# Performance work log

Hardware: AMD Instinct MI355X
Metric: run time of the kernel (lower is better)

The kernel has to match this reference:

```python
import jax, jax.numpy as jnp
import numpy as np

GAMMA = 20.0
GAMMA2 = 10.0
KATZ_FACTOR = 0.999
EPS = 1e-12


def setup_inputs() -> dict:
    key = jax.random.key(0)
    k1, k2 = jax.random.split(key)
    b, n_way, k_shot, q, c, h, w = 32, 5, 5, 75, 640, 5, 5
    support_xf = jax.random.normal(k1, (b, n_way * k_shot, c, h, w), dtype=jnp.float32)
    query_xf = jax.random.normal(k2, (b, q, c, h, w), dtype=jnp.float32)
    return {"support_xf": support_xf, "query_xf": query_xf, "n_way": n_way, "k_shot": k_shot}


def _l2norm(x, axis):
    return x * jax.lax.rsqrt(jnp.sum(x * x, axis=axis, keepdims=True) + EPS)


def reference(support_xf, query_xf, n_way, k_shot):
    b, s, c, h, w = support_xf.shape
    q = query_xf.shape[1]
    hw = h * w
    # prototype support features: mean over shots -> (b, n_way, c, hw)
    sup = support_xf.reshape(b, n_way, k_shot, c, hw).mean(axis=2)
    qry = query_xf.reshape(b, q, c, hw)
    # cosine similarity between every query location and every support location
    sup_n = _l2norm(sup, axis=2)   # (b, n, c, hw)
    qry_n = _l2norm(qry, axis=2)   # (b, q, c, hw)
    # S[b,q,i,n,k]: query pos i vs support (class n, pos k) -> (b*q, M_q, M_s)
    M_q, M_s = hw, n_way * hw
    N = b * q
    S = jnp.einsum('bqci,bnck->bqink', qry_n, sup_n).reshape(N, M_q, M_s)
    # double softmax transition blocks
    T_sq = jax.nn.softmax(GAMMA * S, axis=-1)                    # (N, M_q, M_s)
    T_qs = jax.nn.softmax(GAMMA2 * S.transpose(0, 2, 1), axis=-1)  # (N, M_s, M_q)
    # bipartite block transition matrix T (N, M_s+M_q, M_s+M_q)
    top = jnp.concatenate(
        [jnp.zeros((N, M_s, M_s), S.dtype), T_sq.transpose(0, 2, 1)], axis=-1)
    bot = jnp.concatenate(
        [T_qs.transpose(0, 2, 1), jnp.zeros((N, M_q, M_q), S.dtype)], axis=-1)
    T = jnp.concatenate([top, bot], axis=-2)
    M = M_s + M_q
    eye = jnp.eye(M, dtype=S.dtype)
    ones = jnp.ones((N, M, 1), S.dtype)
    # katz = (inv(I - kT) - I) @ 1 == solve(I - kT, 1) - 1
    katz = (jnp.linalg.solve(eye[None] - KATZ_FACTOR * T, ones) - ones).squeeze(-1)
    kq = katz[:, M_s:]
    ks = katz[:, :M_s]
    katz_query = kq / kq.sum(-1, keepdims=True)
    katz_support = ks / ks.sum(-1, keepdims=True)
    katz_support = katz_support.reshape(b, q, n_way, hw)
    katz_support = katz_support / katz_support.sum(-1, keepdims=True)
    katz_support = katz_support.reshape(b, q, n_way, 1, h, w)
    katz_query = katz_query.reshape(b, q, 1, h, w)
    return (katz_query, katz_support)
```

## Files before the change

### kernel.cpp

```cpp
#include <hip/hip_runtime.h>

namespace {
constexpr int CH = 640, HW = 25, MS = 125;
constexpr int CHW = CH * HW;
constexpr float GAMMA = 20.f, GAMMA2 = 10.f;
constexpr float EPS = 1e-12f;
}

__global__ __launch_bounds__(256)
void prep_sup_kernel(const float* __restrict__ sup, float* __restrict__ sup_t) {
  __shared__ __align__(16) float m[CHW];
  __shared__ float inv[HW];
  const int bn = blockIdx.x;
  const float* base = sup + (size_t)(bn / 5) * (25 * CHW)
                          + (size_t)(bn % 5) * (5 * CHW);
  for (int idx = threadIdx.x; idx < CHW; idx += 256) {
    float s = 0.f;
    #pragma unroll
    for (int sh = 0; sh < 5; ++sh) s += base[sh * CHW + idx];
    m[idx] = s * 0.2f;
  }
  __syncthreads();
  {
    int i = threadIdx.x >> 3, s8 = threadIdx.x & 7;
    if (i < HW) {
      float p = 0.f;
      for (int c = s8; c < CH; c += 8) { float v = m[c * HW + i]; p += v * v; }
      p += __shfl_xor(p, 1); p += __shfl_xor(p, 2); p += __shfl_xor(p, 4);
      if (s8 == 0) inv[i] = rsqrtf(p + EPS);
    }
  }
  __syncthreads();
  float* outp = sup_t + (size_t)bn * CHW;
  for (int idx = threadIdx.x; idx < CHW; idx += 256) {
    int k = idx / CH, c = idx - k * CH;
    outp[idx] = m[c * HW + k] * inv[k];
  }
}

__global__ __launch_bounds__(256)
void gemm_s_kernel(const float* __restrict__ qry, const float* __restrict__ sup_t,
                   float* __restrict__ Sout) {
  __shared__ __align__(16) float pool[4224];
  __shared__ float invq_s[128];
  float* atile = pool;
  float* btile = pool + 2112;

  const int tid = threadIdx.x;
  const int Bl = (blockIdx.x & 7) * 60 + (blockIdx.x >> 3);
  const int b = Bl / 15, qg = Bl - 15 * b;
  const float* qbase = qry + ((size_t)b * 75 + (size_t)qg * 5) * CHW;
  const float* sbase = sup_t + (size_t)b * (MS * CH);
  const int ty = tid >> 4, tx = tid & 15;

  float acc[2][2][4][4];
  #pragma unroll
  for (int g = 0; g < 2; ++g)
    #pragma unroll
    for (int h = 0; h < 2; ++h)
      #pragma unroll
      for (int u = 0; u < 4; ++u)
        #pragma unroll
        for (int v = 0; v < 4; ++v) acc[g][h][u][v] = 0.f;
  float npart = 0.f;

  for (int c0 = 0; c0 < CH; c0 += 16) {
    __syncthreads();
    #pragma unroll
    for (int mm = 0; mm < 8; ++mm) {
      int idx = tid + 256 * mm;
      int k = idx >> 7, row = idx & 127;
      float v = 0.f;
      if (row < MS) {
        int qq = row / 25, i = row - 25 * qq;
        v = qbase[(size_t)qq * CHW + (size_t)(c0 + k) * 25 + i];
      }
      atile[k * 132 + row] = v;
    }
    #pragma unroll
    for (int mm = 0; mm < 2; ++mm) {
      int idx = tid + 256 * mm;
      int col = idx >> 2, kq = idx & 3;
      float4 v = make_float4(0.f, 0.f, 0.f, 0.f);
      if (col < MS) v = *(const float4*)(sbase + (size_t)col * CH + c0 + 4 * kq);
      btile[(4 * kq + 0) * 132 + col] = v.x;
      btile[(4 * kq + 1) * 132 + col] = v.y;
      btile[(4 * kq + 2) * 132 + col] = v.z;
      btile[(4 * kq + 3) * 132 + col] = v.w;
    }
    __syncthreads();
    if (tid < MS) {
      #pragma unroll
      for (int k = 0; k < 16; ++k) { float v = atile[k * 132 + tid]; npart += v * v; }
    }
    #pragma unroll
    for (int k = 0; k < 16; ++k) {
      const float4 a0 = *(const float4*)&atile[k * 132 + 4 * ty];
      const float4 a1 = *(const float4*)&atile[k * 132 + 64 + 4 * ty];
      const float4 b0 = *(const float4*)&btile[k * 132 + 4 * tx];
      const float4 b1 = *(const float4*)&btile[k * 132 + 64 + 4 * tx];
      const float ag[2][4] = {{a0.x, a0.y, a0.z, a0.w}, {a1.x, a1.y, a1.z, a1.w}};
      const float bg[2][4] = {{b0.x, b0.y, b0.z, b0.w}, {b1.x, b1.y, b1.z, b1.w}};
      #pragma unroll
      for (int g = 0; g < 2; ++g)
        #pragma unroll
        for (int u = 0; u < 4; ++u)
          #pragma unroll
          for (int h = 0; h < 2; ++h)
            #pragma unroll
            for (int v = 0; v < 4; ++v) acc[g][h][u][v] += ag[g][u] * bg[h][v];
    }
  }
  if (tid < MS) invq_s[tid] = rsqrtf(npart + EPS);
  __syncthreads();

  float* Sg = Sout + (size_t)(b * 75 + qg * 5) * 3200;
  #pragma unroll
  for (int g = 0; g < 2; ++g)
    #pragma unroll
    for (int u = 0; u < 4; ++u) {
      const int row = g * 64 + 4 * ty + u;
      if (row < MS) {
        const float iv = invq_s[row];
        const int qq = row / 25, r = row - 25 * qq;
        #pragma unroll
        for (int h = 0; h < 2; ++h) {
          float4 val;
          val.x = acc[g][h][u][0] * iv;
          val.y = acc[g][h][u][1] * iv;
          val.z = acc[g][h][u][2] * iv;
          val.w = acc[g][h][u][3] * iv;
          *(float4*)(Sg + (size_t)qq * 3200 + r * 128 + h * 64 + 4 * tx) = val;
        }
      }
    }
}

__global__ __launch_bounds__(256)
void solve_kernel(const float* __restrict__ Sg, float* __restrict__ out) {
  __shared__ float Sld[25 * 131];
  __shared__ float Qm[3125];
  __shared__ double Msol[675];
  __shared__ double xsd[HW];
  __shared__ float kqs[HW];
  __shared__ float ksf[MS];

  const int tid = threadIdx.x;
  const int bq = blockIdx.x;
  const float* src = Sg + (size_t)bq * 3200;
  for (int idx = tid; idx < 3200; idx += 256) {
    const int row = idx >> 7, c = idx & 127;
    Sld[row * 131 + c] = src[idx];
  }
  __syncthreads();

  if (tid < MS) {
    float mx = -1e30f;
    #pragma unroll
    for (int i = 0; i < HW; ++i) mx = fmaxf(mx, Sld[i * 131 + tid]);
    float e[HW]; float sum = 0.f;
    #pragma unroll
    for (int i = 0; i < HW; ++i) { e[i] = __expf(GAMMA2 * (Sld[i * 131 + tid] - mx)); sum += e[i]; }
    float is = 1.f / sum;
    #pragma unroll
    for (int i = 0; i < HW; ++i) Qm[tid * HW + i] = e[i] * is;
  }
  __syncthreads();

  {
    int i = tid >> 3, s8 = tid & 7;
    if (i < HW) {
      float mx = -1e30f;
      for (int j = s8; j < MS; j += 8) mx = fmaxf(mx, Sld[i * 131 + j]);
      mx = fmaxf(mx, __shfl_xor(mx, 1));
      mx = fmaxf(mx, __shfl_xor(mx, 2));
      mx = fmaxf(mx, __shfl_xor(mx, 4));
      float sum = 0.f;
      for (int j = s8; j < MS; j += 8) {
        float e = __expf(GAMMA * (Sld[i * 131 + j] - mx));
        Sld[i * 131 + j] = e; sum += e;
      }
      sum += __shfl_xor(sum, 1); sum += __shfl_xor(sum, 2); sum += __shfl_xor(sum, 4);
      float is = 1.f / sum;
      for (int j = s8; j < MS; j += 8) Sld[i * 131 + j] *= is;
    }
  }
  __syncthreads();

  #pragma unroll
  for (int t = 0; t < 3; ++t) {
    const int pp = tid + 256 * t;
    if (pp < 650) {
      const int i = pp / 26, i2 = pp - 26 * i;
      float s = 0.f;
      if (i2 < 25) {
        for (int j = 0; j < MS; ++j) s += Qm[j * HW + i] * Sld[i2 * 131 + j];
        Msol[i * 27 + i2] = (i == i2 ? 1.0 : 0.0) - 0.998001 * (double)s;
      } else {
        for (int j = 0; j < MS; ++j) s += Qm[j * HW + i];
        Msol[i * 27 + 25] = 1.0 + 0.999 * (double)s;
      }
    }
  }
  __syncthreads();

  for (int k = 0; k < 24; ++k) {
    const double invp = 1.0 / Msol[k * 27 + k];
    const int jj = k + 1 + (tid & 31);
    for (int i = k + 1 + (tid >> 5); i < HW; i += 8) {
      const double f = Msol[i * 27 + k] * invp;
      if (jj <= HW) Msol[i * 27 + jj] -= f * Msol[k * 27 + jj];
    }
    __syncthreads();
  }
  for (int k = 24; k >= 0; --k) {
    const double xk = Msol[k * 27 + 25] / Msol[k * 27 + k];
    if (tid == 0) xsd[k] = xk;
    if (tid < k) Msol[tid * 27 + 25] -= Msol[tid * 27 + k] * xk;
    __syncthreads();
  }

  if (tid < HW) kqs[tid] = (float)(xsd[tid] - 1.0);
  if (tid < MS) {
    float a = 0.f;
    #pragma unroll
    for (int i = 0; i < HW; ++i) a += Sld[i * 131 + tid] * (float)xsd[i];
    ksf[tid] = 0.999f * a;
  }
  __syncthreads();
  if (tid < HW) {
    float s = 0.f;
    #pragma unroll
    for (int i = 0; i < HW; ++i) s += kqs[i];
    out[(size_t)bq * HW + tid] = kqs[tid] / s;
  }
  if (tid < MS) {
    const int n = tid / HW;
    float s = 0.f;
    #pragma unroll
    for (int k2 = 0; k2 < HW; ++k2) s += ksf[n * HW + k2];
    out[60000 + (size_t)bq * MS + tid] = ksf[tid] / s;
  }
}

__global__ __launch_bounds__(256)
void melmask_kernel(const float* __restrict__ qry, const float* __restrict__ sup_t,
                    float* __restrict__ out) {
  __shared__ __align__(16) float pool[4224];
  __shared__ __align__(16) float Sld[3125];
  __shared__ double Msol[675];
  __shared__ double xsd[HW];
  __shared__ float invq_s[128];
  __shared__ float kqs[HW];
  __shared__ float ksf[MS];

  float* atile = pool;
  float* btile = pool + 2112;
  float* Qm    = pool;

  const int tid = threadIdx.x;
  const int Bl = (blockIdx.x & 7) * 60 + (blockIdx.x >> 3);
  const int b = Bl / 15, qg = Bl - 15 * b;
  const float* qbase = qry + ((size_t)b * 75 + (size_t)qg * 5) * CHW;
  const float* sbase = sup_t + (size_t)b * (MS * CH);
  const int ty = tid >> 4, tx = tid & 15;

  float acc[2][2][4][4];
  #pragma unroll
  for (int g = 0; g < 2; ++g)
    #pragma unroll
    for (int h = 0; h < 2; ++h)
      #pragma unroll
      for (int u = 0; u < 4; ++u)
        #pragma unroll
        for (int v = 0; v < 4; ++v) acc[g][h][u][v] = 0.f;
  float npart = 0.f;

  for (int c0 = 0; c0 < CH; c0 += 16) {
    __syncthreads();
    #pragma unroll
    for (int mm = 0; mm < 8; ++mm) {
      int idx = tid + 256 * mm;
      int k = idx >> 7, row = idx & 127;
      float v = 0.f;
      if (row < MS) {
        int qq = row / 25, i = row - 25 * qq;
        v = qbase[(size_t)qq * CHW + (size_t)(c0 + k) * 25 + i];
      }
      atile[k * 132 + row] = v;
    }
    #pragma unroll
    for (int mm = 0; mm < 2; ++mm) {
      int idx = tid + 256 * mm;
      int col = idx >> 2, kq = idx & 3;
      float4 v = make_float4(0.f, 0.f, 0.f, 0.f);
      if (col < MS) v = *(const float4*)(sbase + (size_t)col * CH + c0 + 4 * kq);
      btile[(4 * kq + 0) * 132 + col] = v.x;
      btile[(4 * kq + 1) * 132 + col] = v.y;
      btile[(4 * kq + 2) * 132 + col] = v.z;
      btile[(4 * kq + 3) * 132 + col] = v.w;
    }
    __syncthreads();
    if (tid < MS) {
      #pragma unroll
      for (int k = 0; k < 16; ++k) { float v = atile[k * 132 + tid]; npart += v * v; }
    }
    #pragma unroll
    for (int k = 0; k < 16; ++k) {
      const float4 a0 = *(const float4*)&atile[k * 132 + 4 * ty];
      const float4 a1 = *(const float4*)&atile[k * 132 + 64 + 4 * ty];
      const float4 b0 = *(const float4*)&btile[k * 132 + 4 * tx];
      const float4 b1 = *(const float4*)&btile[k * 132 + 64 + 4 * tx];
      const float ag[2][4] = {{a0.x, a0.y, a0.z, a0.w}, {a1.x, a1.y, a1.z, a1.w}};
      const float bg[2][4] = {{b0.x, b0.y, b0.z, b0.w}, {b1.x, b1.y, b1.z, b1.w}};
      #pragma unroll
      for (int g = 0; g < 2; ++g)
        #pragma unroll
        for (int u = 0; u < 4; ++u)
          #pragma unroll
          for (int h = 0; h < 2; ++h)
            #pragma unroll
            for (int v = 0; v < 4; ++v) acc[g][h][u][v] += ag[g][u] * bg[h][v];
    }
  }
  if (tid < MS) invq_s[tid] = rsqrtf(npart + EPS);
  __syncthreads();

  for (int qq = 0; qq < 5; ++qq) {
    const int bq = b * 75 + qg * 5 + qq;
    const int r0 = qq * 25;
    #pragma unroll
    for (int g = 0; g < 2; ++g)
      #pragma unroll
      for (int u = 0; u < 4; ++u) {
        const int row = g * 64 + 4 * ty + u;
        if (row >= r0 && row < r0 + 25) {
          const int r = row - r0;
          const float iv = invq_s[row];
          #pragma unroll
          for (int h = 0; h < 2; ++h)
            #pragma unroll
            for (int v = 0; v < 4; ++v) {
              const int col = h * 64 + 4 * tx + v;
              if (col < MS) Sld[r * MS + col] = acc[g][h][u][v] * iv;
            }
        }
      }
    __syncthreads();
    if (tid < MS) {
      float mx = -1e30f;
      #pragma unroll
      for (int i = 0; i < HW; ++i) mx = fmaxf(mx, Sld[i * MS + tid]);
      float e[HW]; float sum = 0.f;
      #pragma unroll
      for (int i = 0; i < HW; ++i) { e[i] = __expf(GAMMA2 * (Sld[i * MS + tid] - mx)); sum += e[i]; }
      float is = 1.f / sum;
      #pragma unroll
      for (int i = 0; i < HW; ++i) Qm[tid * HW + i] = e[i] * is;
    }
    __syncthreads();
    {
      int i = tid >> 3, s8 = tid & 7;
      if (i < HW) {
        float mx = -1e30f;
        for (int j = s8; j < MS; j += 8) mx = fmaxf(mx, Sld[i * MS + j]);
        mx = fmaxf(mx, __shfl_xor(mx, 1));
        mx = fmaxf(mx, __shfl_xor(mx, 2));
        mx = fmaxf(mx, __shfl_xor(mx, 4));
        float sum = 0.f;
        for (int j = s8; j < MS; j += 8) {
          float e = __expf(GAMMA * (Sld[i * MS + j] - mx));
          Sld[i * MS + j] = e; sum += e;
        }
        sum += __shfl_xor(sum, 1); sum += __shfl_xor(sum, 2); sum += __shfl_xor(sum, 4);
        float is = 1.f / sum;
        for (int j = s8; j < MS; j += 8) Sld[i * MS + j] *= is;
      }
    }
    __syncthreads();
    float* P = Sld;
    #pragma unroll
    for (int t = 0; t < 3; ++t) {
      const int pp = tid + 256 * t;
      if (pp < 650) {
        const int i = pp / 26, i2 = pp - 26 * i;
        float s = 0.f;
        if (i2 < 25) {
          for (int j = 0; j < MS; ++j) s += Qm[j * HW + i] * P[i2 * MS + j];
          Msol[i * 27 + i2] = (i == i2 ? 1.0 : 0.0) - 0.998001 * (double)s;
        } else {
          for (int j = 0; j < MS; ++j) s += Qm[j * HW + i];
          Msol[i * 27 + 25] = 1.0 + 0.999 * (double)s;
        }
      }
    }
    __syncthreads();
    for (int k = 0; k < 24; ++k) {
      const double invp = 1.0 / Msol[k * 27 + k];
      const int jj = k + 1 + (tid & 31);
      for (int i = k + 1 + (tid >> 5); i < HW; i += 8) {
        const double f = Msol[i * 27 + k] * invp;
        if (jj <= HW) Msol[i * 27 + jj] -= f * Msol[k * 27 + jj];
      }
      __syncthreads();
    }
    for (int k = 24; k >= 0; --k) {
      const double xk = Msol[k * 27 + 25] / Msol[k * 27 + k];
      if (tid == 0) xsd[k] = xk;
      if (tid < k) Msol[tid * 27 + 25] -= Msol[tid * 27 + k] * xk;
      __syncthreads();
    }
    if (tid < HW) kqs[tid] = (float)(xsd[tid] - 1.0);
    if (tid < MS) {
      float a = 0.f;
      #pragma unroll
      for (int i = 0; i < HW; ++i) a += P[i * MS + tid] * (float)xsd[i];
      ksf[tid] = 0.999f * a;
    }
    __syncthreads();
    if (tid < HW) {
      float s = 0.f;
      #pragma unroll
      for (int i = 0; i < HW; ++i) s += kqs[i];
      out[(size_t)bq * HW + tid] = kqs[tid] / s;
    }
    if (tid < MS) {
      const int n = tid / HW;
      float s = 0.f;
      #pragma unroll
      for (int k2 = 0; k2 < HW; ++k2) s += ksf[n * HW + k2];
      out[60000 + (size_t)bq * MS + tid] = ksf[tid] / s;
    }
    __syncthreads();
  }
}

extern "C" void kernel_launch(void* const* d_in, const int* in_sizes, int n_in,
                              void* d_out, int out_size, void* d_ws, size_t ws_size,
                              hipStream_t stream) {
  const float* sup = (const float*)d_in[0];
  const float* qry = (const float*)d_in[1];
  float* outp = (float*)d_out;
  float* sup_t = (float*)d_ws;
  prep_sup_kernel<<<160, 256, 0, stream>>>(sup, sup_t);
  const size_t need = 10240000ull + (size_t)2400 * 3200 * 4;
  if (ws_size >= need) {
    float* Sg = (float*)((char*)d_ws + 10240000);
    gemm_s_kernel<<<480, 256, 0, stream>>>(qry, sup_t, Sg);
    solve_kernel<<<2400, 256, 0, stream>>>(Sg, outp);
  } else {
    melmask_kernel<<<480, 256, 0, stream>>>(qry, sup_t, outp);
  }
}
```

Baseline: 260.7 us.

## Double-buffer GEMM tiles via direct global-to-LDS loads with padded support layout

Adds a support-prep kernel that writes the normalized support as a channel-major, 128-column padded array, so B tiles can be copied with 16-byte direct global-to-LDS loads. The GEMM kernel now double-buffers its A and B tiles in shared memory and prefetches the next channel chunk with global_load_lds while computing the current one. This is meant to overlap global memory latency with FMA work and to remove the register round-trip and transpose stores. The cost is doubled LDS use, which may lower occupancy. A rows beyond 124 are clamped and load duplicate data instead of zeros, which affects only the unused padded rows.

```diff
diff --git a/kernel.cpp b/kernel.cpp
--- a/kernel.cpp
+++ b/kernel.cpp
@@ -8,12 +8,12 @@
 }
 
 __global__ __launch_bounds__(256)
-void prep_sup_kernel(const float* __restrict__ sup, float* __restrict__ sup_t) {
+void prep_sup128_kernel(const float* __restrict__ sup, float* __restrict__ supt) {
   __shared__ __align__(16) float m[CHW];
   __shared__ float inv[HW];
   const int bn = blockIdx.x;
-  const float* base = sup + (size_t)(bn / 5) * (25 * CHW)
-                          + (size_t)(bn % 5) * (5 * CHW);
+  const int b = bn / 5, n = bn % 5;
+  const float* base = sup + ((size_t)b * 25 + n * 5) * CHW;
   for (int idx = threadIdx.x; idx < CHW; idx += 256) {
     float s = 0.f;
     #pragma unroll
@@ -31,6 +31,40 @@
     }
   }
   __syncthreads();
+  float* ob = supt + (size_t)b * (CH * 128);
+  for (int idx = threadIdx.x; idx < CHW; idx += 256) {
+    int c = idx / 25, i = idx - c * 25;
+    ob[c * 128 + n * 25 + i] = m[idx] * inv[i];
+  }
+  if (n == 0)
+    for (int c = threadIdx.x; c < CH; c += 256) {
+      ob[c * 128 + 125] = 0.f; ob[c * 128 + 126] = 0.f; ob[c * 128 + 127] = 0.f;
+    }
+}
+
+__global__ __launch_bounds__(256)
+void prep_sup_kernel(const float* __restrict__ sup, float* __restrict__ sup_t) {
+  __shared__ __align__(16) float m[CHW];
+  __shared__ float inv[HW];
+  const int bn = blockIdx.x;
+  const float* base = sup + (size_t)(bn / 5) * (25 * CHW) + (size_t)(bn % 5) * (5 * CHW);
+  for (int idx = threadIdx.x; idx < CHW; idx += 256) {
+    float s = 0.f;
+    #pragma unroll
+    for (int sh = 0; sh < 5; ++sh) s += base[sh * CHW + idx];
+    m[idx] = s * 0.2f;
+  }
+  __syncthreads();
+  {
+    int i = threadIdx.x >> 3, s8 = threadIdx.x & 7;
+    if (i < HW) {
+      float p = 0.f;
+      for (int c = s8; c < CH; c += 8) { float v = m[c * HW + i]; p += v * v; }
+      p += __shfl_xor(p, 1); p += __shfl_xor(p, 2); p += __shfl_xor(p, 4);
+      if (s8 == 0) inv[i] = rsqrtf(p + EPS);
+    }
+  }
+  __syncthreads();
   float* outp = sup_t + (size_t)bn * CHW;
   for (int idx = threadIdx.x; idx < CHW; idx += 256) {
     int k = idx / CH, c = idx - k * CH;
@@ -39,19 +73,49 @@
 }
 
 __global__ __launch_bounds__(256)
-void gemm_s_kernel(const float* __restrict__ qry, const float* __restrict__ sup_t,
+void gemm_s_kernel(const float* __restrict__ qry, const float* __restrict__ sup128,
                    float* __restrict__ Sout) {
-  __shared__ __align__(16) float pool[4224];
+  __shared__ __align__(16) float atile[2][16 * 128];
+  __shared__ __align__(16) float btile[2][16 * 128];
   __shared__ float invq_s[128];
-  float* atile = pool;
-  float* btile = pool + 2112;
 
   const int tid = threadIdx.x;
+  const int wid = tid >> 6, lane = tid & 63;
   const int Bl = (blockIdx.x & 7) * 60 + (blockIdx.x >> 3);
   const int b = Bl / 15, qg = Bl - 15 * b;
   const float* qbase = qry + ((size_t)b * 75 + (size_t)qg * 5) * CHW;
-  const float* sbase = sup_t + (size_t)b * (MS * CH);
+  const float* sb = sup128 + (size_t)b * (CH * 128);
   const int ty = tid >> 4, tx = tid & 15;
+
+  const int row0 = lane;
+  const int qq0 = row0 / 25, i0 = row0 - 25 * qq0;
+  int row1 = 64 + lane; if (row1 > 124) row1 = 124;
+  const int qq1 = row1 / 25, i1 = row1 - 25 * qq1;
+  const size_t aoff0 = (size_t)qq0 * CHW + i0;
+  const size_t aoff1 = (size_t)qq1 * CHW + i1;
+
+  auto STAGE = [&](int pp, int c0) {
+    float* at = atile[pp];
+    float* bt = btile[pp];
+    #pragma unroll
+    for (int rr = 0; rr < 8; ++rr) {
+      const int r = 8 * wid + rr;
+      const int k = r >> 1;
+      const size_t aoff = (r & 1) ? aoff1 : aoff0;
+      const float* src = qbase + aoff + (size_t)(c0 + k) * 25;
+      __builtin_amdgcn_global_load_lds(
+          (const __attribute__((address_space(1))) void*)src,
+          (__attribute__((address_space(3))) void*)(at + r * 64), 4, 0, 0);
+    }
+    #pragma unroll
+    for (int jj = 0; jj < 2; ++jj) {
+      const int j = 2 * wid + jj;
+      const float* src = sb + (size_t)(c0 + 2 * j) * 128 + lane * 4;
+      __builtin_amdgcn_global_load_lds(
+          (const __attribute__((address_space(1))) void*)src,
+          (__attribute__((address_space(3))) void*)(bt + j * 256), 16, 0, 0);
+    }
+  };
 
   float acc[2][2][4][4];
   #pragma unroll
@@ -64,41 +128,25 @@
         for (int v = 0; v < 4; ++v) acc[g][h][u][v] = 0.f;
   float npart = 0.f;
 
-  for (int c0 = 0; c0 < CH; c0 += 16) {
-    __syncthreads();
-    #pragma unroll
-    for (int mm = 0; mm < 8; ++mm) {
-      int idx = tid + 256 * mm;
-      int k = idx >> 7, row = idx & 127;
-      float v = 0.f;
-      if (row < MS) {
-        int qq = row / 25, i = row - 25 * qq;
-        v = qbase[(size_t)qq * CHW + (size_t)(c0 + k) * 25 + i];
-      }
-      atile[k * 132 + row] = v;
-    }
-    #pragma unroll
-    for (int mm = 0; mm < 2; ++mm) {
-      int idx = tid + 256 * mm;
-      int col = idx >> 2, kq = idx & 3;
-      float4 v = make_float4(0.f, 0.f, 0.f, 0.f);
-      if (col < MS) v = *(const float4*)(sbase + (size_t)col * CH + c0 + 4 * kq);
-      btile[(4 * kq + 0) * 132 + col] = v.x;
-      btile[(4 * kq + 1) * 132 + col] = v.y;
-      btile[(4 * kq + 2) * 132 + col] = v.z;
-      btile[(4 * kq + 3) * 132 + col] = v.w;
-    }
-    __syncthreads();
+  STAGE(0, 0);
+  asm volatile("s_waitcnt vmcnt(0)" ::: "memory");
+  __syncthreads();
+
+  int p = 0;
+  for (int t = 0; t < 40; ++t) {
+    if (t < 39) STAGE(p ^ 1, 16 * (t + 1));
+    const float* at = atile[p];
+    const float* bt = btile[p];
     if (tid < MS) {
       #pragma unroll
-      for (int k = 0; k < 16; ++k) { float v = atile[k * 132 + tid]; npart += v * v; }
+      for (int k = 0; k < 16; ++k) { float v = at[k * 128 + tid]; npart += v * v; }
     }
     #pragma unroll
     for (int k = 0; k < 16; ++k) {
-      const float4 a0 = *(const float4*)&atile[k * 132 + 4 * ty];
-      const float4 a1 = *(const float4*)&atile[k * 132 + 64 + 4 * ty];
-      const float4 b0 = *(const float4*)&btile[k * 132 + 4 * tx];
-      const float4 b1 = *(const float4*)&btile[k * 132 + 64 + 4 * tx];
+      const float4 a0 = *(const float4*)&at[k * 128 + 4 * ty];
+      const float4 a1 = *(const float4*)&at[k * 128 + 64 + 4 * ty];
+      const float4 b0 = *(const float4*)&bt[k * 128 + 4 * tx];
+      const float4 b1 = *(const float4*)&bt[k * 128 + 64 + 4 * tx];
       const float ag[2][4] = {{a0.x, a0.y, a0.z, a0.w}, {a1.x, a1.y, a1.z, a1.w}};
       const float bg[2][4] = {{b0.x, b0.y, b0.z, b0.w}, {b1.x, b1.y, b1.z, b1.w}};
       #pragma unroll
@@ -110,6 +158,9 @@
             #pragma unroll
             for (int v = 0; v < 4; ++v) acc[g][h][u][v] += ag[g][u] * bg[h][v];
     }
+    asm volatile("s_waitcnt vmcnt(0)" ::: "memory");
+    __syncthreads();
+    p ^= 1;
   }
   if (tid < MS) invq_s[tid] = rsqrtf(npart + EPS);
   __syncthreads();
@@ -441,14 +492,17 @@
   const float* sup = (const float*)d_in[0];
   const float* qry = (const float*)d_in[1];
   float* outp = (float*)d_out;
-  float* sup_t = (float*)d_ws;
-  prep_sup_kernel<<<160, 256, 0, stream>>>(sup, sup_t);
-  const size_t need = 10240000ull + (size_t)2400 * 3200 * 4;
-  if (ws_size >= need) {
-    float* Sg = (float*)((char*)d_ws + 10240000);
-    gemm_s_kernel<<<480, 256, 0, stream>>>(qry, sup_t, Sg);
+  const size_t sup128_bytes = (size_t)32 * CH * 128 * 4;
+  const size_t sg_bytes = (size_t)2400 * 3200 * 4;
+  if (ws_size >= sup128_bytes + sg_bytes) {
+    float* sup128 = (float*)d_ws;
+    float* Sg = (float*)((char*)d_ws + sup128_bytes);
+    prep_sup128_kernel<<<160, 256, 0, stream>>>(sup, sup128);
+    gemm_s_kernel<<<480, 256, 0, stream>>>(qry, sup128, Sg);
     solve_kernel<<<2400, 256, 0, stream>>>(Sg, outp);
   } else {
+    float* sup_t = (float*)d_ws;
+    prep_sup_kernel<<<160, 256, 0, stream>>>(sup, sup_t);
     melmask_kernel<<<480, 256, 0, stream>>>(qry, sup_t, outp);
   }
 }
```

Result: faster. 243.1 us, median of 3 (-6.7%).
